# Performance work log

Measured on AMD Instinct MI355X. Metric: run time of the kernel, lower is better.

## Reference

```python
import jax, jax.numpy as jnp
import numpy as np
import itertools

GRID = 256          # voxel grid extent per axis (coords in [0, GRID))
KSIZE = 3           # kernel_size
OFFSETS = np.array(list(itertools.product(range(KSIZE), repeat=3)), dtype=np.int32) - (KSIZE // 2)  # [27,3]


def setup_inputs() -> dict:
    key = jax.random.key(0)
    k1, k2, k3 = jax.random.split(key, 3)
    N, Cin, Cout = 262144, 64, 64
    coords = jax.random.randint(k1, (N, 3), 0, GRID, dtype=jnp.int32)
    feats = jax.random.normal(k2, (N, Cin), dtype=jnp.float32)
    kernel = jax.random.normal(k3, (KSIZE ** 3, Cin, Cout), dtype=jnp.float32) * 0.02
    return {"coords": coords, "feats": feats, "kernel": kernel}


def reference(coords, feats, kernel):
    # Submanifold sparse conv3d: out[i] = sum_k feats[j_k(i)] @ kernel[k]
    # where coords[j_k(i)] == coords[i] + offset_k (if such a point exists).
    N = coords.shape[0]
    Cout = kernel.shape[-1]
    # Hash table: linearized voxel -> point index (-1 if empty).
    lin = (coords[:, 0] * GRID + coords[:, 1]) * GRID + coords[:, 2]
    table = jnp.full((GRID ** 3,), -1, dtype=jnp.int32).at[lin].set(
        jnp.arange(N, dtype=jnp.int32))
    out = jnp.zeros((N, Cout), dtype=feats.dtype)
    for k in range(KSIZE ** 3):
        off = jnp.asarray(OFFSETS[k])              # [3]
        nc = coords + off[None, :]                 # neighbor coords [N,3]
        in_bounds = jnp.all((nc >= 0) & (nc < GRID), axis=1)
        nlin = (nc[:, 0] * GRID + nc[:, 1]) * GRID + nc[:, 2]
        idx = table[jnp.clip(nlin, 0, GRID ** 3 - 1)]
        valid = in_bounds & (idx >= 0)
        g = feats[jnp.where(valid, idx, 0)] * valid[:, None].astype(feats.dtype)  # [N,Cin]
        out = out + g @ kernel[k]                  # [N,Cout]
    return out
```

## Files before the change

### kernel.cpp

```cpp
#include <hip/hip_runtime.h>

#define VGRID 256
#define N_TAPS 27
#define CIN 64
#define COUT 64
#define PAIR_CAP 16384
#define CNT_STRIDE 16
#define LCAP 64

typedef short short8 __attribute__((ext_vector_type(8)));
typedef float float4v __attribute__((ext_vector_type(4)));

__device__ __forceinline__ short f2bf(float x) {
    unsigned u = __builtin_bit_cast(unsigned, x);
    unsigned r = (u + 0x7FFF + ((u >> 16) & 1)) >> 16;
    return (short)r;
}

__global__ void build_table_kernel(const int* __restrict__ coords,
                                   int* __restrict__ table,
                                   unsigned* __restrict__ bits, int n) {
    int i = blockIdx.x * blockDim.x + threadIdx.x;
    if (i >= n) return;
    int lin = (coords[i * 3 + 0] * VGRID + coords[i * 3 + 1]) * VGRID + coords[i * 3 + 2];
    atomicMax(&table[lin], i);
    atomicOr(&bits[lin >> 5], 1u << (lin & 31));
}

__global__ void wconvert_kernel(const float* __restrict__ W,
                                short* __restrict__ Wt) {
    int tap = blockIdx.x;
    for (int e = threadIdx.x; e < CIN * COUT; e += 256) {
        int ci = e >> 6, co = e & 63;
        Wt[((size_t)tap * COUT + co) * CIN + ci] = f2bf(W[((size_t)tap * CIN + ci) * COUT + co]);
    }
}

__global__ void __launch_bounds__(256) probe_kernel(
        const int* __restrict__ coords, const int* __restrict__ table,
        const unsigned* __restrict__ bits,
        int* __restrict__ counters, int2* __restrict__ pairs,
        int* __restrict__ jc, int n) {
    __shared__ int lcnt[26];
    __shared__ int lbase[26];
    __shared__ int2 lpairs[26][LCAP];

    int t = threadIdx.x;
    int i = blockIdx.x * 256 + t;
    if (t < 26) lcnt[t] = 0;
    __syncthreads();

    int cx = 0, cy = 0, cz = 0;
    unsigned hitmask = 0;
    if (i < n) {
        cx = coords[i * 3 + 0];
        cy = coords[i * 3 + 1];
        cz = coords[i * 3 + 2];

        int clin = (cx * VGRID + cy) * VGRID + cz;
        int center_idx = table[clin];

        unsigned w[N_TAPS];
#pragma unroll
        for (int k = 0; k < N_TAPS; ++k) {
            int ox = k / 9 - 1, oy = (k / 3) % 3 - 1, oz = k % 3 - 1;
            int nx = cx + ox, ny = cy + oy, nz = cz + oz;
            bool v = ((unsigned)nx < VGRID) && ((unsigned)ny < VGRID) &&
                     ((unsigned)nz < VGRID);
            int nlin = (nx * VGRID + ny) * VGRID + nz;
            w[k] = v ? bits[(unsigned)nlin >> 5] : 0u;
        }
#pragma unroll
        for (int k = 0; k < N_TAPS; ++k) {
            if (k == 13) continue;
            int nz = cz + (k % 3 - 1);
            if ((w[k] >> (nz & 31)) & 1u) hitmask |= 1u << k;
        }
        jc[i] = center_idx;
    }

    while (__builtin_amdgcn_ballot_w64(hitmask != 0)) {
        if (hitmask) {
            int k = __builtin_ctz(hitmask);
            hitmask &= hitmask - 1;
            int ox = k / 9 - 1, oy = (k / 3) % 3 - 1, oz = k % 3 - 1;
            int nlin = ((cx + ox) * VGRID + (cy + oy)) * VGRID + (cz + oz);
            int idx = table[nlin];
            int kidx = k - (k > 13);
            int pos = atomicAdd(&lcnt[kidx], 1);
            if (pos < LCAP) lpairs[kidx][pos] = make_int2(i, idx);
        }
    }
    __syncthreads();

    if (t < 26) {
        int c = lcnt[t];
        if (c > LCAP) c = LCAP;
        lcnt[t] = c;
        lbase[t] = atomicAdd(&counters[t * CNT_STRIDE], c);
    }
    __syncthreads();

    int wave = t >> 6, lane = t & 63;
    for (int k = wave; k < 26; k += 4) {
        int c = lcnt[k];
        if (lane < c) {
            int pos = lbase[k] + lane;
            if (pos < PAIR_CAP) pairs[(size_t)k * PAIR_CAP + pos] = lpairs[k][lane];
        }
    }
}

__global__ void __launch_bounds__(256) center_gemm_kernel(
        const float* __restrict__ feats, const short* __restrict__ Wt,
        const int* __restrict__ jc, float* __restrict__ out, int n) {
    __shared__ short a_lds[64][CIN + 8];
    int base = blockIdx.x * 64;
    int t = threadIdx.x;

    {
        int r = t >> 2;
        int seg = (t & 3) * 16;
        int row = base + r;
        int j = (row < n) ? jc[row] : 0;
        const float4* src = (const float4*)(feats + (size_t)j * CIN + seg);
#pragma unroll
        for (int q = 0; q < 4; ++q) {
            float4 v = src[q];
            a_lds[r][seg + q * 4 + 0] = f2bf(v.x);
            a_lds[r][seg + q * 4 + 1] = f2bf(v.y);
            a_lds[r][seg + q * 4 + 2] = f2bf(v.z);
            a_lds[r][seg + q * 4 + 3] = f2bf(v.w);
        }
    }
    __syncthreads();

    int wave = t >> 6, lane = t & 63;
    int quad = lane >> 4, m = lane & 15;
    const short* W13 = Wt + 13 * CIN * COUT;
    int row0 = wave * 16;

#pragma unroll
    for (int nt = 0; nt < 4; ++nt) {
        float4v acc = {0.f, 0.f, 0.f, 0.f};
        int nn = nt * 16 + m;
#pragma unroll
        for (int ks = 0; ks < 2; ++ks) {
            short8 a = *(const short8*)&a_lds[row0 + m][ks * 32 + quad * 8];
            short8 b = *(const short8*)(W13 + (size_t)nn * CIN + ks * 32 + quad * 8);
            acc = __builtin_amdgcn_mfma_f32_16x16x32_bf16(a, b, acc, 0, 0, 0);
        }
#pragma unroll
        for (int r2 = 0; r2 < 4; ++r2) {
            int orow = base + row0 + quad * 4 + r2;
            if (orow < n) out[(size_t)orow * COUT + nn] = acc[r2];
        }
    }
}

__global__ void __launch_bounds__(256) scatter_gemm_kernel(
        const float* __restrict__ feats, const short* __restrict__ Wt,
        const int* __restrict__ counters, const int2* __restrict__ pairs,
        float* __restrict__ out) {
    __shared__ short a_lds[64][CIN + 8];
    __shared__ int i_arr[64];

    int kidx = blockIdx.y;
    int tap = kidx + (kidx >= 13);
    int cnt = counters[kidx * CNT_STRIDE];
    if (cnt > PAIR_CAP) cnt = PAIR_CAP;
    int ntiles = (cnt + 63) >> 6;
    const short* W = Wt + (size_t)tap * CIN * COUT;
    const int2* P = pairs + (size_t)kidx * PAIR_CAP;

    int t = threadIdx.x;
    int wave = t >> 6, lane = t & 63;
    int quad = lane >> 4, m = lane & 15;

    for (int tile = blockIdx.x; tile < ntiles; tile += gridDim.x) {
        int tbase = tile * 64;
        int rem = cnt - tbase;
        if (rem > 64) rem = 64;

        if (t < 64) i_arr[t] = (t < rem) ? P[tbase + t].x : -1;
        {
            int r = t >> 2;
            int seg = (t & 3) * 16;
            int j = (r < rem) ? P[tbase + r].y : -1;
#pragma unroll
            for (int q = 0; q < 4; ++q) {
                float4 v = {0.f, 0.f, 0.f, 0.f};
                if (j >= 0) v = *(const float4*)(feats + (size_t)j * CIN + seg + q * 4);
                a_lds[r][seg + q * 4 + 0] = f2bf(v.x);
                a_lds[r][seg + q * 4 + 1] = f2bf(v.y);
                a_lds[r][seg + q * 4 + 2] = f2bf(v.z);
                a_lds[r][seg + q * 4 + 3] = f2bf(v.w);
            }
        }
        __syncthreads();

        int row0 = wave * 16;
#pragma unroll
        for (int nt = 0; nt < 4; ++nt) {
            float4v acc = {0.f, 0.f, 0.f, 0.f};
            int nn = nt * 16 + m;
#pragma unroll
            for (int ks = 0; ks < 2; ++ks) {
                short8 a = *(const short8*)&a_lds[row0 + m][ks * 32 + quad * 8];
                short8 b = *(const short8*)(W + (size_t)nn * CIN + ks * 32 + quad * 8);
                acc = __builtin_amdgcn_mfma_f32_16x16x32_bf16(a, b, acc, 0, 0, 0);
            }
#pragma unroll
            for (int r2 = 0; r2 < 4; ++r2) {
                int i = i_arr[row0 + quad * 4 + r2];
                if (i >= 0) atomicAdd(&out[(size_t)i * COUT + nn], acc[r2]);
            }
        }
        __syncthreads();
    }
}

extern "C" void kernel_launch(void* const* d_in, const int* in_sizes, int n_in,
                              void* d_out, int out_size, void* d_ws, size_t ws_size,
                              hipStream_t stream) {
    const int* coords = (const int*)d_in[0];
    const float* feats = (const float*)d_in[1];
    const float* weights = (const float*)d_in[2];
    float* out = (float*)d_out;

    int n = in_sizes[0] / 3;

    char* ws = (char*)d_ws;
    size_t BITMAP_BYTES = (size_t)VGRID * VGRID * VGRID / 8;
    unsigned* bits = (unsigned*)ws;
    int* counters = (int*)(ws + BITMAP_BYTES);
    short* wbft = (short*)(ws + BITMAP_BYTES + 4096);
    int* jc = (int*)(ws + BITMAP_BYTES + 4096 + 221184);
    int2* pairs = (int2*)(ws + BITMAP_BYTES + 4096 + 221184 + (size_t)n * 4);
    int* table = (int*)(ws + BITMAP_BYTES + 4096 + 221184 + (size_t)n * 4
                        + (size_t)26 * PAIR_CAP * 8);

    hipMemsetAsync(ws, 0, BITMAP_BYTES + 4096, stream);

    int blocks = (n + 255) / 256;
    build_table_kernel<<<blocks, 256, 0, stream>>>(coords, table, bits, n);
    wconvert_kernel<<<N_TAPS, 256, 0, stream>>>(weights, wbft);
    probe_kernel<<<blocks, 256, 0, stream>>>(coords, table, bits, counters, pairs, jc, n);

    int cg_blocks = (n + 63) / 64;
    center_gemm_kernel<<<cg_blocks, 256, 0, stream>>>(feats, wbft, jc, out, n);

    dim3 sg_grid(96, 26);
    scatter_gemm_kernel<<<sg_grid, 256, 0, stream>>>(feats, wbft, counters, pairs, out);
}
```

Before: 227.0 us.

## Fuse weight conversion into table build and center GEMM into probe kernel

Merges the weight bf16 conversion into the table-build launch as extra blocks, and folds the center-tap GEMM into the probe kernel so the center indices stay in shared memory instead of going through a global jc buffer. This removes two kernel launches and a global write/read of the center index array. In exchange, the probe kernel uses more shared memory and has a longer serial tail per block, which may reduce occupancy and overlap.

```diff
diff --git a/kernel.cpp b/kernel.cpp
--- a/kernel.cpp
+++ b/kernel.cpp
@@ -17,33 +17,37 @@
     return (short)r;
 }
 
-__global__ void build_table_kernel(const int* __restrict__ coords,
-                                   int* __restrict__ table,
-                                   unsigned* __restrict__ bits, int n) {
-    int i = blockIdx.x * blockDim.x + threadIdx.x;
+__global__ void __launch_bounds__(256) build_kernel(
+        const int* __restrict__ coords, int* __restrict__ table,
+        unsigned* __restrict__ bits, const float* __restrict__ W,
+        short* __restrict__ Wt, int n, int bt_blocks) {
+    if ((int)blockIdx.x >= bt_blocks) {
+        int tap = blockIdx.x - bt_blocks;
+        for (int e = threadIdx.x; e < CIN * COUT; e += 256) {
+            int ci = e >> 6, co = e & 63;
+            Wt[((size_t)tap * COUT + co) * CIN + ci] =
+                f2bf(W[((size_t)tap * CIN + ci) * COUT + co]);
+        }
+        return;
+    }
+    int i = blockIdx.x * 256 + threadIdx.x;
     if (i >= n) return;
     int lin = (coords[i * 3 + 0] * VGRID + coords[i * 3 + 1]) * VGRID + coords[i * 3 + 2];
     atomicMax(&table[lin], i);
     atomicOr(&bits[lin >> 5], 1u << (lin & 31));
 }
 
-__global__ void wconvert_kernel(const float* __restrict__ W,
-                                short* __restrict__ Wt) {
-    int tap = blockIdx.x;
-    for (int e = threadIdx.x; e < CIN * COUT; e += 256) {
-        int ci = e >> 6, co = e & 63;
-        Wt[((size_t)tap * COUT + co) * CIN + ci] = f2bf(W[((size_t)tap * CIN + ci) * COUT + co]);
-    }
-}
-
-__global__ void __launch_bounds__(256) probe_kernel(
+__global__ void __launch_bounds__(256) probe_center_kernel(
         const int* __restrict__ coords, const int* __restrict__ table,
         const unsigned* __restrict__ bits,
         int* __restrict__ counters, int2* __restrict__ pairs,
-        int* __restrict__ jc, int n) {
+        const float* __restrict__ feats, const short* __restrict__ Wt,
+        float* __restrict__ out, int n) {
     __shared__ int lcnt[26];
     __shared__ int lbase[26];
     __shared__ int2 lpairs[26][LCAP];
+    __shared__ int jc_s[256];
+    __shared__ short a_lds[64][CIN + 8];
 
     int t = threadIdx.x;
     int i = blockIdx.x * 256 + t;
@@ -52,13 +56,13 @@
 
     int cx = 0, cy = 0, cz = 0;
     unsigned hitmask = 0;
+    int center_idx = 0;
     if (i < n) {
         cx = coords[i * 3 + 0];
         cy = coords[i * 3 + 1];
         cz = coords[i * 3 + 2];
-
         int clin = (cx * VGRID + cy) * VGRID + cz;
-        int center_idx = table[clin];
+        center_idx = table[clin];
 
         unsigned w[N_TAPS];
 #pragma unroll
@@ -76,8 +80,8 @@
             int nz = cz + (k % 3 - 1);
             if ((w[k] >> (nz & 31)) & 1u) hitmask |= 1u << k;
         }
-        jc[i] = center_idx;
-    }
+    }
+    jc_s[t] = center_idx;
 
     while (__builtin_amdgcn_ballot_w64(hitmask != 0)) {
         if (hitmask) {
@@ -109,51 +113,46 @@
             if (pos < PAIR_CAP) pairs[(size_t)k * PAIR_CAP + pos] = lpairs[k][lane];
         }
     }
-}
-
-__global__ void __launch_bounds__(256) center_gemm_kernel(
-        const float* __restrict__ feats, const short* __restrict__ Wt,
-        const int* __restrict__ jc, float* __restrict__ out, int n) {
-    __shared__ short a_lds[64][CIN + 8];
-    int base = blockIdx.x * 64;
-    int t = threadIdx.x;
-
-    {
-        int r = t >> 2;
-        int seg = (t & 3) * 16;
-        int row = base + r;
-        int j = (row < n) ? jc[row] : 0;
-        const float4* src = (const float4*)(feats + (size_t)j * CIN + seg);
-#pragma unroll
-        for (int q = 0; q < 4; ++q) {
-            float4 v = src[q];
-            a_lds[r][seg + q * 4 + 0] = f2bf(v.x);
-            a_lds[r][seg + q * 4 + 1] = f2bf(v.y);
-            a_lds[r][seg + q * 4 + 2] = f2bf(v.z);
-            a_lds[r][seg + q * 4 + 3] = f2bf(v.w);
-        }
-    }
-    __syncthreads();
-
-    int wave = t >> 6, lane = t & 63;
+
     int quad = lane >> 4, m = lane & 15;
     const short* W13 = Wt + 13 * CIN * COUT;
-    int row0 = wave * 16;
-
-#pragma unroll
-    for (int nt = 0; nt < 4; ++nt) {
-        float4v acc = {0.f, 0.f, 0.f, 0.f};
-        int nn = nt * 16 + m;
-#pragma unroll
-        for (int ks = 0; ks < 2; ++ks) {
-            short8 a = *(const short8*)&a_lds[row0 + m][ks * 32 + quad * 8];
-            short8 b = *(const short8*)(W13 + (size_t)nn * CIN + ks * 32 + quad * 8);
-            acc = __builtin_amdgcn_mfma_f32_16x16x32_bf16(a, b, acc, 0, 0, 0);
-        }
-#pragma unroll
-        for (int r2 = 0; r2 < 4; ++r2) {
-            int orow = base + row0 + quad * 4 + r2;
-            if (orow < n) out[(size_t)orow * COUT + nn] = acc[r2];
+    int base = blockIdx.x * 256;
+
+    for (int rt = 0; rt < 4; ++rt) {
+        __syncthreads();
+        {
+            int r = t >> 2;
+            int seg = (t & 3) * 16;
+            int grow = base + rt * 64 + r;
+            int j = (grow < n) ? jc_s[rt * 64 + r] : 0;
+            const float4* src = (const float4*)(feats + (size_t)j * CIN + seg);
+#pragma unroll
+            for (int q = 0; q < 4; ++q) {
+                float4 v = src[q];
+                a_lds[r][seg + q * 4 + 0] = f2bf(v.x);
+                a_lds[r][seg + q * 4 + 1] = f2bf(v.y);
+                a_lds[r][seg + q * 4 + 2] = f2bf(v.z);
+                a_lds[r][seg + q * 4 + 3] = f2bf(v.w);
+            }
+        }
+        __syncthreads();
+
+        int row0 = wave * 16;
+#pragma unroll
+        for (int nt = 0; nt < 4; ++nt) {
+            float4v acc = {0.f, 0.f, 0.f, 0.f};
+            int nn = nt * 16 + m;
+#pragma unroll
+            for (int ks = 0; ks < 2; ++ks) {
+                short8 a = *(const short8*)&a_lds[row0 + m][ks * 32 + quad * 8];
+                short8 b = *(const short8*)(W13 + (size_t)nn * CIN + ks * 32 + quad * 8);
+                acc = __builtin_amdgcn_mfma_f32_16x16x32_bf16(a, b, acc, 0, 0, 0);
+            }
+#pragma unroll
+            for (int r2 = 0; r2 < 4; ++r2) {
+                int orow = base + rt * 64 + row0 + quad * 4 + r2;
+                if (orow < n) out[(size_t)orow * COUT + nn] = acc[r2];
+            }
         }
     }
 }
@@ -235,20 +234,19 @@
     unsigned* bits = (unsigned*)ws;
     int* counters = (int*)(ws + BITMAP_BYTES);
     short* wbft = (short*)(ws + BITMAP_BYTES + 4096);
-    int* jc = (int*)(ws + BITMAP_BYTES + 4096 + 221184);
-    int2* pairs = (int2*)(ws + BITMAP_BYTES + 4096 + 221184 + (size_t)n * 4);
-    int* table = (int*)(ws + BITMAP_BYTES + 4096 + 221184 + (size_t)n * 4
+    int2* pairs = (int2*)(ws + BITMAP_BYTES + 4096 + 221184);
+    int* table = (int*)(ws + BITMAP_BYTES + 4096 + 221184
                         + (size_t)26 * PAIR_CAP * 8);
 
     hipMemsetAsync(ws, 0, BITMAP_BYTES + 4096, stream);
 
-    int blocks = (n + 255) / 256;
-    build_table_kernel<<<blocks, 256, 0, stream>>>(coords, table, bits, n);
-    wconvert_kernel<<<N_TAPS, 256, 0, stream>>>(weights, wbft);
-    probe_kernel<<<blocks, 256, 0, stream>>>(coords, table, bits, counters, pairs, jc, n);
-
-    int cg_blocks = (n + 63) / 64;
-    center_gemm_kernel<<<cg_blocks, 256, 0, stream>>>(feats, wbft, jc, out, n);
+    int bt_blocks = (n + 255) / 256;
+    build_kernel<<<bt_blocks + N_TAPS, 256, 0, stream>>>(coords, table, bits,
+                                                         weights, wbft, n, bt_blocks);
+
+    probe_center_kernel<<<bt_blocks, 256, 0, stream>>>(coords, table, bits,
+                                                       counters, pairs, feats,
+                                                       wbft, out, n);
 
     dim3 sg_grid(96, 26);
     scatter_gemm_kernel<<<sg_grid, 256, 0, stream>>>(feats, wbft, counters, pairs, out);
```

Result: faster. 215.5 us (-5.1%).
